# Kernel tuning notes

Hardware: AMD Instinct MI355X
Metric: run time of the kernel (lower is better)

## Reference

```python
import jax, jax.numpy as jnp
import numpy as np

ALPHA = 0.1
THETA = 0.5
N_NODES = 50000
N_EDGES = 320000
IN_F, HID, OUT_F, N_LAYERS = 50, 256, 121, 4


def setup_inputs() -> dict:
    key = jax.random.key(0)
    ks = jax.random.split(key, 8)
    x = jax.random.normal(ks[0], (N_NODES, IN_F), dtype=jnp.float32)
    edge_index = jax.random.randint(ks[1], (2, N_EDGES), 0, N_NODES, dtype=jnp.int64)
    edge_weight = jax.random.uniform(ks[2], (N_EDGES,), dtype=jnp.float32) / 8.0  # ~normalized adj values
    lin0_w = jax.random.normal(ks[3], (IN_F, HID), dtype=jnp.float32) / np.sqrt(IN_F)
    lin0_b = jnp.zeros((HID,), dtype=jnp.float32)
    W = jax.random.normal(ks[4], (N_LAYERS, HID, HID), dtype=jnp.float32) / np.sqrt(HID)
    lin1_w = jax.random.normal(ks[5], (HID, OUT_F), dtype=jnp.float32) / np.sqrt(HID)
    lin1_b = jnp.zeros((OUT_F,), dtype=jnp.float32)
    return {"x": x, "edge_index": edge_index, "edge_weight": edge_weight,
            "lin0_w": lin0_w, "lin0_b": lin0_b, "W": W,
            "lin1_w": lin1_w, "lin1_b": lin1_b}


def reference(x, edge_index, edge_weight, lin0_w, lin0_b, W, lin1_w, lin1_b):
    # Eval mode: dropout is identity.
    n = x.shape[0]
    src, dst = edge_index[0], edge_index[1]
    x0 = jax.nn.relu(x @ lin0_w + lin0_b)          # [N, H] initial residual
    h = x0
    for l in range(W.shape[0]):
        beta = jnp.log(THETA / (l + 1) + 1.0)       # GCN2Conv beta, layer = l+1
        # sparse adj propagation: agg[i] = sum_{e: dst=i} w_e * h[src_e]
        agg = jax.ops.segment_sum(edge_weight[:, None] * h[src], dst, num_segments=n)
        s = (1.0 - ALPHA) * agg + ALPHA * x0        # initial-residual mixing
        out = (1.0 - beta) * s + beta * (s @ W[l])  # identity-mapped weight (shared)
        h = jax.nn.relu(out + h)                    # outer residual + relu
    return h @ lin1_w + lin1_b                      # [N, num_classes]
```

## Files before the change

kernel.cpp:

```cpp
#include <hip/hip_runtime.h>
#include <math.h>

#define IN_F   50
#define HID    256
#define OUT_F  121
#define N_LAYERS 4
#define K0PAD  64

typedef __attribute__((ext_vector_type(8))) short short8;
typedef __attribute__((ext_vector_type(4))) float f32x4;

#define GLOBAL_AS __attribute__((address_space(1)))
#define LDS_AS    __attribute__((address_space(3)))

__device__ __forceinline__ ushort f2bf(float f) {
    union { float f; unsigned u; } c; c.f = f;
    unsigned u = c.u;
    u += 0x7fffu + ((u >> 16) & 1u);
    return (ushort)(u >> 16);
}
__device__ __forceinline__ float bf2f(ushort u) {
    union { unsigned u; float f; } c; c.u = ((unsigned)u) << 16;
    return c.f;
}

__global__ __launch_bounds__(256) void prep_kernel(
        const float* __restrict__ x, const float* __restrict__ w0,
        const float* __restrict__ W, const float* __restrict__ w1,
        ushort* __restrict__ x_bf, ushort* __restrict__ wt0,
        ushort* __restrict__ Wt, ushort* __restrict__ wt1,
        int* __restrict__ counts, int n) {
    long long flat = (long long)blockIdx.x * 256 + threadIdx.x;
    long long r0 = (long long)n * K0PAD;
    if (flat < r0) {
        int nd = (int)(flat >> 6), k = (int)(flat & 63);
        x_bf[flat] = (k < IN_F) ? f2bf(x[(size_t)nd * IN_F + k]) : 0;
        return;
    }
    flat -= r0;
    if (flat < HID * K0PAD) {
        int nn = (int)(flat >> 6), k = (int)(flat & 63);
        wt0[flat] = (k < IN_F) ? f2bf(w0[(size_t)k * HID + nn]) : 0;
        return;
    }
    flat -= HID * K0PAD;
    if (flat < N_LAYERS * HID * HID) {
        int l = (int)(flat >> 16);
        int rem = (int)(flat & 65535);
        int ts = rem >> 13;
        int kq = (rem >> 11) & 3;
        int nn = (rem >> 3) & 255;
        int j  = rem & 7;
        int k  = ts * 32 + kq * 8 + j;
        float beta = logf(0.5f / (float)(l + 1) + 1.0f);
        float v = beta * W[(size_t)l * HID * HID + (size_t)k * HID + nn];
        if (k == nn) v += 1.0f - beta;
        Wt[flat] = f2bf(v);
        return;
    }
    flat -= N_LAYERS * HID * HID;
    if (flat < 128 * HID) {
        int nn = (int)(flat >> 8), k = (int)(flat & 255);
        wt1[flat] = (nn < OUT_F) ? f2bf(w1[(size_t)k * OUT_F + nn]) : 0;
        return;
    }
    flat -= 128 * HID;
    if (flat < n) counts[flat] = 0;
}

__global__ void hist_kernel(const int* __restrict__ dst, int* __restrict__ counts, int E) {
    int e = blockIdx.x * blockDim.x + threadIdx.x;
    if (e < E) atomicAdd(&counts[dst[e]], 1);
}

__global__ void scan_phase1(const int* __restrict__ counts, int* __restrict__ row_ptr,
                            int* __restrict__ bsum, int n) {
    __shared__ int sd[1024];
    int t = threadIdx.x;
    int i = blockIdx.x * 1024 + t;
    int v = (i < n) ? counts[i] : 0;
    sd[t] = v;
    __syncthreads();
    for (int off = 1; off < 1024; off <<= 1) {
        int tmp = (t >= off) ? sd[t - off] : 0;
        __syncthreads();
        sd[t] += tmp;
        __syncthreads();
    }
    if (i < n) row_ptr[i] = sd[t] - v;
    if (t == 1023) bsum[blockIdx.x] = sd[1023];
}

__global__ void scan_phase2(int* __restrict__ bsum, int nb) {
    __shared__ int sd[64];
    int t = threadIdx.x;
    int v = (t < nb) ? bsum[t] : 0;
    sd[t] = v;
    __syncthreads();
    for (int off = 1; off < 64; off <<= 1) {
        int tmp = (t >= off) ? sd[t - off] : 0;
        __syncthreads();
        sd[t] += tmp;
        __syncthreads();
    }
    if (t < nb) bsum[t] = sd[t] - v;
    if (t == nb - 1) bsum[nb] = sd[t];
}

__global__ void scan_phase3(int* __restrict__ row_ptr, int* __restrict__ cursor,
                            const int* __restrict__ bsum, int n, int nb) {
    int i = blockIdx.x * 1024 + threadIdx.x;
    if (i < n) {
        int v = row_ptr[i] + bsum[blockIdx.x];
        row_ptr[i] = v;
        cursor[i]  = v;
    }
    if (i == n - 1) row_ptr[n] = bsum[nb];
}

__global__ void scatter_kernel(const int* __restrict__ src, const int* __restrict__ dst,
                               const float* __restrict__ ew, int* __restrict__ cursor,
                               int* __restrict__ col, float* __restrict__ wv, int E) {
    int e = blockIdx.x * blockDim.x + threadIdx.x;
    if (e < E) {
        int d = dst[e];
        int pos = atomicAdd(&cursor[d], 1);
        col[pos] = src[e];
        wv[pos] = ew[e];
    }
}

__global__ __launch_bounds__(256) void lin0_mfma(
        const ushort* __restrict__ x_bf, const ushort* __restrict__ wt0,
        const float* __restrict__ b, ushort* __restrict__ x0_bf,
        ushort* __restrict__ h_bf, int M) {
    __shared__ ushort As[4][128][8];
    __shared__ ushort Bs[4][128][8];
    int tid = threadIdx.x;
    int wave = tid >> 6;
    int lane = tid & 63;
    int r16 = lane & 15, q = lane >> 4;
    int bm = blockIdx.x * 128;
    int bn = blockIdx.y * 128;
    int wm = (wave >> 1) * 64, wn = (wave & 1) * 64;

    f32x4 acc[4][4] = {};

    int srow = tid & 127;
    int koff0 = tid >> 7;
    int arow = bm + srow; if (arow >= M) arow = M - 1;
    const ushort* aptr = x_bf + (size_t)arow * K0PAD;
    const ushort* bptr = wt0 + (size_t)(bn + srow) * K0PAD;
    char* AsB = (char*)&As[0][0][0];
    char* BsB = (char*)&Bs[0][0][0];
    int woff = wave * 1024;

    const short8* As8 = (const short8*)&As[0][0][0];
    const short8* Bs8 = (const short8*)&Bs[0][0][0];

    for (int k0 = 0; k0 < K0PAD; k0 += 32) {
        __builtin_amdgcn_global_load_lds((const GLOBAL_AS void*)(aptr + k0 + koff0 * 8),
                                         (LDS_AS void*)(AsB + woff), 16, 0, 0);
        __builtin_amdgcn_global_load_lds((const GLOBAL_AS void*)(aptr + k0 + (koff0 + 2) * 8),
                                         (LDS_AS void*)(AsB + 4096 + woff), 16, 0, 0);
        __builtin_amdgcn_global_load_lds((const GLOBAL_AS void*)(bptr + k0 + koff0 * 8),
                                         (LDS_AS void*)(BsB + woff), 16, 0, 0);
        __builtin_amdgcn_global_load_lds((const GLOBAL_AS void*)(bptr + k0 + (koff0 + 2) * 8),
                                         (LDS_AS void*)(BsB + 4096 + woff), 16, 0, 0);
        __syncthreads();

        short8 av[4], bv[4];
#pragma unroll
        for (int mf = 0; mf < 4; ++mf)
            av[mf] = As8[q * 128 + wm + mf * 16 + r16];
#pragma unroll
        for (int nf = 0; nf < 4; ++nf)
            bv[nf] = Bs8[q * 128 + wn + nf * 16 + r16];
#pragma unroll
        for (int mf = 0; mf < 4; ++mf)
#pragma unroll
            for (int nf = 0; nf < 4; ++nf)
                acc[mf][nf] = __builtin_amdgcn_mfma_f32_16x16x32_bf16(av[mf], bv[nf], acc[mf][nf], 0, 0, 0);
        __syncthreads();
    }

#pragma unroll
    for (int mf = 0; mf < 4; ++mf) {
#pragma unroll
        for (int j = 0; j < 4; ++j) {
            int row = bm + wm + mf * 16 + q * 4 + j;
            if (row >= M) continue;
#pragma unroll
            for (int nf = 0; nf < 4; ++nf) {
                int c = bn + wn + nf * 16 + r16;
                size_t idx = (size_t)row * HID + c;
                ushort v = f2bf(fmaxf(acc[mf][nf][j] + b[c], 0.f));
                x0_bf[idx] = v;
                h_bf[idx]  = v;
            }
        }
    }
}

__global__ __launch_bounds__(256) void spmm_mix_kernel(
        const int* __restrict__ row_ptr, const int* __restrict__ col,
        const float* __restrict__ wv, const ushort* __restrict__ h_bf,
        const ushort* __restrict__ x0_bf, ushort* __restrict__ s_bf, int n) {
    int node = (blockIdx.x * 256 + threadIdx.x) >> 6;
    if (node >= n) return;
    int lane = threadIdx.x & 63;
    int f0 = lane * 4;
    int beg = row_ptr[node], end = row_ptr[node + 1];
    float a0 = 0.f, a1 = 0.f, a2 = 0.f, a3 = 0.f;
    int e = beg;
    for (; e + 4 <= end; e += 4) {
        int c0 = col[e], c1 = col[e + 1], c2 = col[e + 2], c3 = col[e + 3];
        float w0 = wv[e], w1 = wv[e + 1], w2 = wv[e + 2], w3 = wv[e + 3];
        ushort4 v0 = *reinterpret_cast<const ushort4*>(&h_bf[(size_t)c0 * HID + f0]);
        ushort4 v1 = *reinterpret_cast<const ushort4*>(&h_bf[(size_t)c1 * HID + f0]);
        ushort4 v2 = *reinterpret_cast<const ushort4*>(&h_bf[(size_t)c2 * HID + f0]);
        ushort4 v3 = *reinterpret_cast<const ushort4*>(&h_bf[(size_t)c3 * HID + f0]);
        a0 = fmaf(w0, bf2f(v0.x), a0); a1 = fmaf(w0, bf2f(v0.y), a1);
        a2 = fmaf(w0, bf2f(v0.z), a2); a3 = fmaf(w0, bf2f(v0.w), a3);
        a0 = fmaf(w1, bf2f(v1.x), a0); a1 = fmaf(w1, bf2f(v1.y), a1);
        a2 = fmaf(w1, bf2f(v1.z), a2); a3 = fmaf(w1, bf2f(v1.w), a3);
        a0 = fmaf(w2, bf2f(v2.x), a0); a1 = fmaf(w2, bf2f(v2.y), a1);
        a2 = fmaf(w2, bf2f(v2.z), a2); a3 = fmaf(w2, bf2f(v2.w), a3);
        a0 = fmaf(w3, bf2f(v3.x), a0); a1 = fmaf(w3, bf2f(v3.y), a1);
        a2 = fmaf(w3, bf2f(v3.z), a2); a3 = fmaf(w3, bf2f(v3.w), a3);
    }
    if (e + 2 <= end) {
        int c0 = col[e], c1 = col[e + 1];
        float w0 = wv[e], w1 = wv[e + 1];
        ushort4 v0 = *reinterpret_cast<const ushort4*>(&h_bf[(size_t)c0 * HID + f0]);
        ushort4 v1 = *reinterpret_cast<const ushort4*>(&h_bf[(size_t)c1 * HID + f0]);
        a0 = fmaf(w0, bf2f(v0.x), a0); a1 = fmaf(w0, bf2f(v0.y), a1);
        a2 = fmaf(w0, bf2f(v0.z), a2); a3 = fmaf(w0, bf2f(v0.w), a3);
        a0 = fmaf(w1, bf2f(v1.x), a0); a1 = fmaf(w1, bf2f(v1.y), a1);
        a2 = fmaf(w1, bf2f(v1.z), a2); a3 = fmaf(w1, bf2f(v1.w), a3);
        e += 2;
    }
    if (e < end) {
        int c0 = col[e];
        float w0 = wv[e];
        ushort4 v0 = *reinterpret_cast<const ushort4*>(&h_bf[(size_t)c0 * HID + f0]);
        a0 = fmaf(w0, bf2f(v0.x), a0); a1 = fmaf(w0, bf2f(v0.y), a1);
        a2 = fmaf(w0, bf2f(v0.z), a2); a3 = fmaf(w0, bf2f(v0.w), a3);
    }
    size_t idx = (size_t)node * HID + f0;
    ushort4 xv = *reinterpret_cast<const ushort4*>(&x0_bf[idx]);
    ushort4 r;
    r.x = f2bf(0.9f * a0 + 0.1f * bf2f(xv.x));
    r.y = f2bf(0.9f * a1 + 0.1f * bf2f(xv.y));
    r.z = f2bf(0.9f * a2 + 0.1f * bf2f(xv.z));
    r.w = f2bf(0.9f * a3 + 0.1f * bf2f(xv.w));
    *reinterpret_cast<ushort4*>(&s_bf[idx]) = r;
}

__global__ __launch_bounds__(512) void gemm_mfma_layer(
        const ushort* __restrict__ s_bf, const ushort* __restrict__ wt,
        ushort* __restrict__ h_bf, int M) {
    __shared__ ushort As[128 * 32];
    __shared__ ushort Bs[4 * 256 * 8];
    int tid = threadIdx.x;
    int wave = tid >> 6;
    int lane = tid & 63;
    int r16 = lane & 15, q = lane >> 4;
    int bm = blockIdx.x * 128;
    int wm = (wave >> 2) * 64, wn = (wave & 3) * 64;

    f32x4 acc[4][4] = {};

    int arow_l = tid >> 2;
    int p = tid & 3;
    int gsrc = p ^ ((arow_l >> 1) & 3);
    int arow = bm + arow_l; if (arow >= M) arow = M - 1;
    const ushort* aptr = s_bf + (size_t)arow * HID;
    char* AsB = (char*)As;
    char* BsB = (char*)Bs;
    const short8* Bs8 = (const short8*)Bs;

    for (int ts = 0; ts < 8; ++ts) {
        __builtin_amdgcn_global_load_lds((const GLOBAL_AS void*)(aptr + ts * 32 + gsrc * 8),
                                         (LDS_AS void*)(AsB + tid * 16), 16, 0, 0);
        __builtin_amdgcn_global_load_lds((const GLOBAL_AS void*)(wt + (size_t)ts * 8192 + tid * 8),
                                         (LDS_AS void*)(BsB + tid * 16), 16, 0, 0);
        __builtin_amdgcn_global_load_lds((const GLOBAL_AS void*)(wt + (size_t)ts * 8192 + (tid + 512) * 8),
                                         (LDS_AS void*)(BsB + (tid + 512) * 16), 16, 0, 0);
        __syncthreads();

        short8 av[4], bv[4];
#pragma unroll
        for (int mf = 0; mf < 4; ++mf) {
            int row = wm + mf * 16 + r16;
            int g = q ^ ((row >> 1) & 3);
            av[mf] = *reinterpret_cast<const short8*>(AsB + row * 64 + g * 16);
        }
#pragma unroll
        for (int nf = 0; nf < 4; ++nf)
            bv[nf] = Bs8[q * 256 + wn + nf * 16 + r16];
#pragma unroll
        for (int mf = 0; mf < 4; ++mf)
#pragma unroll
            for (int nf = 0; nf < 4; ++nf)
                acc[mf][nf] = __builtin_amdgcn_mfma_f32_16x16x32_bf16(av[mf], bv[nf], acc[mf][nf], 0, 0, 0);
        __syncthreads();
    }

#pragma unroll
    for (int mf = 0; mf < 4; ++mf) {
#pragma unroll
        for (int j = 0; j < 4; ++j) {
            int row = bm + wm + mf * 16 + q * 4 + j;
            if (row >= M) continue;
#pragma unroll
            for (int nf = 0; nf < 4; ++nf) {
                int c = wn + nf * 16 + r16;
                size_t idx = (size_t)row * HID + c;
                float v = fmaxf(acc[mf][nf][j] + bf2f(h_bf[idx]), 0.f);
                h_bf[idx] = f2bf(v);
            }
        }
    }
}

__global__ __launch_bounds__(256) void lin1_mfma(
        const ushort* __restrict__ h_bf, const ushort* __restrict__ wt1,
        const float* __restrict__ b, float* __restrict__ out, int M) {
    __shared__ ushort As[4][128][8];
    __shared__ ushort Bs[4][128][8];
    int tid = threadIdx.x;
    int wave = tid >> 6;
    int lane = tid & 63;
    int r16 = lane & 15, q = lane >> 4;
    int bm = blockIdx.x * 128;
    int wm = (wave >> 1) * 64, wn = (wave & 1) * 64;

    f32x4 acc[4][4] = {};

    int srow = tid & 127;
    int koff0 = tid >> 7;
    int arow = bm + srow; if (arow >= M) arow = M - 1;
    const ushort* aptr = h_bf + (size_t)arow * HID;
    const ushort* bptr = wt1 + (size_t)srow * HID;
    char* AsB = (char*)&As[0][0][0];
    char* BsB = (char*)&Bs[0][0][0];
    int woff = wave * 1024;

    const short8* As8 = (const short8*)&As[0][0][0];
    const short8* Bs8 = (const short8*)&Bs[0][0][0];

    for (int k0 = 0; k0 < HID; k0 += 32) {
        __builtin_amdgcn_global_load_lds((const GLOBAL_AS void*)(aptr + k0 + koff0 * 8),
                                         (LDS_AS void*)(AsB + woff), 16, 0, 0);
        __builtin_amdgcn_global_load_lds((const GLOBAL_AS void*)(aptr + k0 + (koff0 + 2) * 8),
                                         (LDS_AS void*)(AsB + 4096 + woff), 16, 0, 0);
        __builtin_amdgcn_global_load_lds((const GLOBAL_AS void*)(bptr + k0 + koff0 * 8),
                                         (LDS_AS void*)(BsB + woff), 16, 0, 0);
        __builtin_amdgcn_global_load_lds((const GLOBAL_AS void*)(bptr + k0 + (koff0 + 2) * 8),
                                         (LDS_AS void*)(BsB + 4096 + woff), 16, 0, 0);
        __syncthreads();

        short8 av[4], bv[4];
#pragma unroll
        for (int mf = 0; mf < 4; ++mf)
            av[mf] = As8[q * 128 + wm + mf * 16 + r16];
#pragma unroll
        for (int nf = 0; nf < 4; ++nf)
            bv[nf] = Bs8[q * 128 + wn + nf * 16 + r16];
#pragma unroll
        for (int mf = 0; mf < 4; ++mf)
#pragma unroll
            for (int nf = 0; nf < 4; ++nf)
                acc[mf][nf] = __builtin_amdgcn_mfma_f32_16x16x32_bf16(av[mf], bv[nf], acc[mf][nf], 0, 0, 0);
        __syncthreads();
    }

#pragma unroll
    for (int mf = 0; mf < 4; ++mf) {
#pragma unroll
        for (int j = 0; j < 4; ++j) {
            int row = bm + wm + mf * 16 + q * 4 + j;
            if (row >= M) continue;
#pragma unroll
            for (int nf = 0; nf < 4; ++nf) {
                int c = wn + nf * 16 + r16;
                if (c < OUT_F)
                    out[(size_t)row * OUT_F + c] = acc[mf][nf][j] + b[c];
            }
        }
    }
}

extern "C" void kernel_launch(void* const* d_in, const int* in_sizes, int n_in,
                              void* d_out, int out_size, void* d_ws, size_t ws_size,
                              hipStream_t stream) {
    const float* x      = (const float*)d_in[0];
    const int*   ei     = (const int*)d_in[1];
    const float* ew     = (const float*)d_in[2];
    const float* lin0_w = (const float*)d_in[3];
    const float* lin0_b = (const float*)d_in[4];
    const float* W      = (const float*)d_in[5];
    const float* lin1_w = (const float*)d_in[6];
    const float* lin1_b = (const float*)d_in[7];
    float* out = (float*)d_out;

    int N = in_sizes[0] / IN_F;
    int E = in_sizes[2];
    const int* src = ei;
    const int* dst = ei + E;

    char* ws = (char*)d_ws;
    ushort* x0_bf   = (ushort*)ws; ws += (size_t)N * HID * 2;
    ushort* h_bf    = (ushort*)ws; ws += (size_t)N * HID * 2;
    ushort* s_bf    = (ushort*)ws; ws += (size_t)N * HID * 2;
    ushort* x_bf    = (ushort*)ws; ws += (size_t)N * K0PAD * 2;
    ushort* Wt0     = (ushort*)ws; ws += (size_t)HID * K0PAD * 2;
    ushort* Wt      = (ushort*)ws; ws += (size_t)N_LAYERS * HID * HID * 2;
    ushort* Wt1     = (ushort*)ws; ws += (size_t)128 * HID * 2;
    int*    row_ptr = (int*)ws;    ws += (size_t)(N + 1) * 4;
    int*    counts  = (int*)ws;    ws += (size_t)N * 4;
    int*    cursor  = (int*)ws;    ws += (size_t)N * 4;
    int*    bsum    = (int*)ws;    ws += (size_t)128 * 4;
    int*    col     = (int*)ws;    ws += (size_t)E * 4;
    float*  wv      = (float*)ws;  ws += (size_t)E * 4;

    int nb = (N + 1023) / 1024;

    size_t prep_tot = (size_t)N * K0PAD + HID * K0PAD
                    + (size_t)N_LAYERS * HID * HID + 128 * HID + N;
    prep_kernel<<<(int)((prep_tot + 255) / 256), 256, 0, stream>>>(
        x, lin0_w, W, lin1_w, x_bf, Wt0, Wt, Wt1, counts, N);

    hist_kernel<<<(E + 255) / 256, 256, 0, stream>>>(dst, counts, E);
    scan_phase1<<<nb, 1024, 0, stream>>>(counts, row_ptr, bsum, N);
    scan_phase2<<<1, 64, 0, stream>>>(bsum, nb);
    scan_phase3<<<nb, 1024, 0, stream>>>(row_ptr, cursor, bsum, N, nb);
    scatter_kernel<<<(E + 255) / 256, 256, 0, stream>>>(src, dst, ew, cursor, col, wv, E);

    int mblocks = (N + 127) / 128;
    lin0_mfma<<<dim3(mblocks, 2), 256, 0, stream>>>(x_bf, Wt0, lin0_b, x0_bf, h_bf, N);

    for (int l = 0; l < N_LAYERS; ++l) {
        spmm_mix_kernel<<<(N + 3) / 4, 256, 0, stream>>>(row_ptr, col, wv, h_bf, x0_bf, s_bf, N);
        gemm_mfma_layer<<<mblocks, 512, 0, stream>>>(
            s_bf, Wt + (size_t)l * HID * HID, h_bf, N);
    }

    lin1_mfma<<<mblocks, 256, 0, stream>>>(h_bf, Wt1, lin1_b, out, N);
}
```

Measured before the change: 292.4 us.

## Add double-buffered layer GEMM and fold block-sum scan into phase3

Adds a double-buffered variant of the per-layer MFMA GEMM that prefetches the next K-slice into LDS via global_load_lds while the current slice is computed, and uses it for layers 2 and 3 only. It also removes the scan_phase2 launch by having each phase3 block serially prefix-sum the block sums in shared memory. The aim is to hide global load latency in the GEMM and drop one kernel launch. The cost is twice the LDS per block, which may lower occupancy, plus redundant serial work in every phase3 block. Using the new GEMM for only half the layers looks like an A/B experiment.

```diff
diff --git a/kernel.cpp b/kernel.cpp
--- a/kernel.cpp
+++ b/kernel.cpp
@@ -91,31 +91,23 @@
     if (t == 1023) bsum[blockIdx.x] = sd[1023];
 }
 
-__global__ void scan_phase2(int* __restrict__ bsum, int nb) {
-    __shared__ int sd[64];
-    int t = threadIdx.x;
-    int v = (t < nb) ? bsum[t] : 0;
-    sd[t] = v;
-    __syncthreads();
-    for (int off = 1; off < 64; off <<= 1) {
-        int tmp = (t >= off) ? sd[t - off] : 0;
-        __syncthreads();
-        sd[t] += tmp;
-        __syncthreads();
-    }
-    if (t < nb) bsum[t] = sd[t] - v;
-    if (t == nb - 1) bsum[nb] = sd[t];
-}
-
 __global__ void scan_phase3(int* __restrict__ row_ptr, int* __restrict__ cursor,
                             const int* __restrict__ bsum, int n, int nb) {
-    int i = blockIdx.x * 1024 + threadIdx.x;
+    __shared__ int pref[129];
+    int t = threadIdx.x;
+    if (t == 0) {
+        int run = 0;
+        for (int b = 0; b < nb; ++b) { pref[b] = run; run += bsum[b]; }
+        pref[nb] = run;
+    }
+    __syncthreads();
+    int i = blockIdx.x * 1024 + t;
     if (i < n) {
-        int v = row_ptr[i] + bsum[blockIdx.x];
+        int v = row_ptr[i] + pref[blockIdx.x];
         row_ptr[i] = v;
         cursor[i]  = v;
     }
-    if (i == n - 1) row_ptr[n] = bsum[nb];
+    if (blockIdx.x == 0 && t == 0) row_ptr[n] = pref[nb];
 }
 
 __global__ void scatter_kernel(const int* __restrict__ src, const int* __restrict__ dst,
@@ -324,6 +316,84 @@
     }
 }
 
+__global__ __launch_bounds__(512) void gemm_mfma_layer_db(
+        const ushort* __restrict__ s_bf, const ushort* __restrict__ wt,
+        ushort* __restrict__ h_bf, int M) {
+    __shared__ ushort As[2][128 * 32];
+    __shared__ ushort Bs[2][4 * 256 * 8];
+    int tid = threadIdx.x;
+    int wave = tid >> 6;
+    int lane = tid & 63;
+    int r16 = lane & 15, q = lane >> 4;
+    int bm = blockIdx.x * 128;
+    int wm = (wave >> 2) * 64, wn = (wave & 3) * 64;
+
+    f32x4 acc[4][4] = {};
+
+    int arow_l = tid >> 2;
+    int p = tid & 3;
+    int gsrc = p ^ ((arow_l >> 1) & 3);
+    int arow = bm + arow_l; if (arow >= M) arow = M - 1;
+    const ushort* aptr = s_bf + (size_t)arow * HID;
+
+#define STAGE_DB(buf, ts)                                                                  \
+    __builtin_amdgcn_global_load_lds((const GLOBAL_AS void*)(aptr + (ts) * 32 + gsrc * 8), \
+                                     (LDS_AS void*)((char*)As[buf] + tid * 16), 16, 0, 0); \
+    __builtin_amdgcn_global_load_lds((const GLOBAL_AS void*)(wt + (size_t)(ts) * 8192 + tid * 8), \
+                                     (LDS_AS void*)((char*)Bs[buf] + tid * 16), 16, 0, 0); \
+    __builtin_amdgcn_global_load_lds((const GLOBAL_AS void*)(wt + (size_t)(ts) * 8192 + (tid + 512) * 8), \
+                                     (LDS_AS void*)((char*)Bs[buf] + (tid + 512) * 16), 16, 0, 0);
+
+    STAGE_DB(0, 0);
+#pragma unroll
+    for (int ts = 0; ts < 8; ++ts) {
+        const int cur = ts & 1;
+        if (ts < 7) { STAGE_DB(cur ^ 1, ts + 1); }
+        if (ts < 7) asm volatile("s_waitcnt vmcnt(3)" ::: "memory");
+        else        asm volatile("s_waitcnt vmcnt(0)" ::: "memory");
+        __builtin_amdgcn_s_barrier();
+        asm volatile("" ::: "memory");
+
+        const char* AsB = (const char*)As[cur];
+        const short8* Bs8 = (const short8*)Bs[cur];
+        short8 av[4], bv[4];
+#pragma unroll
+        for (int mf = 0; mf < 4; ++mf) {
+            int row = wm + mf * 16 + r16;
+            int g = q ^ ((row >> 1) & 3);
+            av[mf] = *reinterpret_cast<const short8*>(AsB + row * 64 + g * 16);
+        }
+#pragma unroll
+        for (int nf = 0; nf < 4; ++nf)
+            bv[nf] = Bs8[q * 256 + wn + nf * 16 + r16];
+#pragma unroll
+        for (int mf = 0; mf < 4; ++mf)
+#pragma unroll
+            for (int nf = 0; nf < 4; ++nf)
+                acc[mf][nf] = __builtin_amdgcn_mfma_f32_16x16x32_bf16(av[mf], bv[nf], acc[mf][nf], 0, 0, 0);
+
+        asm volatile("" ::: "memory");
+        __builtin_amdgcn_s_barrier();
+    }
+#undef STAGE_DB
+
+#pragma unroll
+    for (int mf = 0; mf < 4; ++mf) {
+#pragma unroll
+        for (int j = 0; j < 4; ++j) {
+            int row = bm + wm + mf * 16 + q * 4 + j;
+            if (row >= M) continue;
+#pragma unroll
+            for (int nf = 0; nf < 4; ++nf) {
+                int c = wn + nf * 16 + r16;
+                size_t idx = (size_t)row * HID + c;
+                float v = fmaxf(acc[mf][nf][j] + bf2f(h_bf[idx]), 0.f);
+                h_bf[idx] = f2bf(v);
+            }
+        }
+    }
+}
+
 __global__ __launch_bounds__(256) void lin1_mfma(
         const ushort* __restrict__ h_bf, const ushort* __restrict__ wt1,
         const float* __restrict__ b, float* __restrict__ out, int M) {
@@ -434,7 +504,6 @@
 
     hist_kernel<<<(E + 255) / 256, 256, 0, stream>>>(dst, counts, E);
     scan_phase1<<<nb, 1024, 0, stream>>>(counts, row_ptr, bsum, N);
-    scan_phase2<<<1, 64, 0, stream>>>(bsum, nb);
     scan_phase3<<<nb, 1024, 0, stream>>>(row_ptr, cursor, bsum, N, nb);
     scatter_kernel<<<(E + 255) / 256, 256, 0, stream>>>(src, dst, ew, cursor, col, wv, E);
 
@@ -443,8 +512,12 @@
 
     for (int l = 0; l < N_LAYERS; ++l) {
         spmm_mix_kernel<<<(N + 3) / 4, 256, 0, stream>>>(row_ptr, col, wv, h_bf, x0_bf, s_bf, N);
-        gemm_mfma_layer<<<mblocks, 512, 0, stream>>>(
-            s_bf, Wt + (size_t)l * HID * HID, h_bf, N);
+        if (l < 2)
+            gemm_mfma_layer<<<mblocks, 512, 0, stream>>>(
+                s_bf, Wt + (size_t)l * HID * HID, h_bf, N);
+        else
+            gemm_mfma_layer_db<<<mblocks, 512, 0, stream>>>(
+                s_bf, Wt + (size_t)l * HID * HID, h_bf, N);
     }
 
     lin1_mfma<<<mblocks, 256, 0, stream>>>(h_bf, Wt1, lin1_b, out, N);
```

Result: no change. 289.5 us (-1.0%).
